# Kernel optimization log

Hardware: AMD Instinct MI355X
Metric: run time of the kernel (lower is better)

Reference implementation:

```python
import jax, jax.numpy as jnp
import numpy as np
import itertools
from jax import lax

B, CIN, COUT, RES, NH = 32, 512, 512, 56, 8
STRIDE = RES // 7  # 8 -> post-stride grid is 7x7 (N=49)
HD = COUT // NH    # 64


def _affine(x, s, b):  # BatchNorm2d in inference form (per-channel scale/shift)
    return x * s[None, :, None, None] + b[None, :, None, None]


def _conv1x1(x, w):  # w: [O, C]
    return jnp.einsum('oc,bchw->bohw', w, x)


def _conv3x3(x, w, stride, groups):
    return lax.conv_general_dilated(
        x, w, window_strides=(stride, stride), padding=[(1, 1), (1, 1)],
        feature_group_count=groups, dimension_numbers=('NCHW', 'OIHW', 'NCHW'))


def _bias_idx():
    points = list(itertools.product(range(7), range(7)))
    offsets, idxs = {}, []
    for p1 in points:
        for p2 in points:
            off = (abs(p1[0] - p2[0]), abs(p1[1] - p2[1]))
            if off not in offsets:
                offsets[off] = len(offsets)
            idxs.append(offsets[off])
    return np.array(idxs, dtype=np.int32).reshape(49, 49), len(offsets)


def setup_inputs() -> dict:
    key = jax.random.key(0)
    ks = jax.random.split(key, 24)
    idx_np, n_off = _bias_idx()  # n_off = 49
    rn = lambda k, sh, sc: jax.random.normal(k, sh, dtype=jnp.float32) * sc
    return {
        'x': rn(ks[0], (B, CIN, RES, RES), 1.0),
        'dw_w': rn(ks[1], (CIN, 1, 3, 3), 0.2),
        'bn0_s': 1.0 + rn(ks[2], (CIN,), 0.05), 'bn0_b': rn(ks[3], (CIN,), 0.05),
        'wq': rn(ks[4], (COUT, CIN), 0.03),
        'bnq_s': 1.0 + rn(ks[5], (COUT,), 0.05), 'bnq_b': rn(ks[6], (COUT,), 0.05),
        'wk': rn(ks[7], (COUT, CIN), 0.03),
        'bnk_s': 1.0 + rn(ks[8], (COUT,), 0.05), 'bnk_b': rn(ks[9], (COUT,), 0.05),
        'wv': rn(ks[10], (COUT, CIN), 0.03),
        'bnv_s': 1.0 + rn(ks[11], (COUT,), 0.05), 'bnv_b': rn(ks[12], (COUT,), 0.05),
        'loc_w': rn(ks[13], (COUT, COUT // NH, 3, 3), 0.05), 'loc_b': rn(ks[14], (COUT,), 0.02),
        'bnl_s': 1.0 + rn(ks[15], (COUT,), 0.05), 'bnl_b': rn(ks[16], (COUT,), 0.05),
        'th1': rn(ks[17], (NH, NH), 0.3), 'th2': rn(ks[18], (NH, NH), 0.3),
        'logit_scale': jnp.log(10.0) * jnp.ones((NH, 1, 1), dtype=jnp.float32),
        'ab': rn(ks[19], (NH, n_off), 0.02),
        'wo': rn(ks[20], (COUT, COUT), 0.03),
        'bno_s': 1.0 + rn(ks[21], (COUT,), 0.05), 'bno_b': rn(ks[22], (COUT,), 0.05),
        'bias_idx': jnp.array(idx_np),
    }


def reference(x, dw_w, bn0_s, bn0_b, wq, bnq_s, bnq_b, wk, bnk_s, bnk_b,
              wv, bnv_s, bnv_b, loc_w, loc_b, bnl_s, bnl_b, th1, th2,
              logit_scale, ab, wo, bno_s, bno_b, bias_idx):
    # stride_conv: depthwise 3x3 stride-8 + BN -> [B, C, 7, 7]
    x = _affine(_conv3x3(x, dw_w, STRIDE, CIN), bn0_s, bn0_b)
    Bc, C, H, W = x.shape
    N = H * W  # 49
    q = _affine(_conv1x1(x, wq), bnq_s, bnq_b).reshape(Bc, NH, HD, N).transpose(0, 1, 3, 2)  # [B,H,N,d]
    k = _affine(_conv1x1(x, wk), bnk_s, bnk_b).reshape(Bc, NH, HD, N)                        # [B,H,d,N]
    v4 = _affine(_conv1x1(x, wv), bnv_s, bnv_b)                                              # [B,Cout,7,7]
    v_local = _affine(_conv3x3(v4, loc_w, 1, NH) + loc_b[None, :, None, None], bnl_s, bnl_b)
    v = v4.reshape(Bc, NH, HD, N).transpose(0, 1, 3, 2)                                      # [B,H,N,d]
    # faithful to source: q normalized over head_dim, k normalized over token axis (last)
    qn = q / jnp.maximum(jnp.linalg.norm(q, axis=-1, keepdims=True), 1e-12)
    kn = k / jnp.maximum(jnp.linalg.norm(k, axis=-1, keepdims=True), 1e-12)
    ls = jnp.exp(jnp.minimum(logit_scale, jnp.log(100.0)))  # clamp max then exp
    attn = jnp.einsum('bhnd,bhdm->bhnm', qn, kn) * ls + ab[:, bias_idx]  # [B,H,49,49]
    attn = jnp.einsum('ij,bjnm->binm', th1, attn)   # talking head 1
    attn = jax.nn.softmax(attn, axis=-1)
    attn = jnp.einsum('ij,bjnm->binm', th2, attn)   # talking head 2
    out = jnp.einsum('bhnm,bhmd->bhnd', attn, v)    # [B,H,N,d]
    out = out.transpose(0, 1, 3, 2).reshape(Bc, COUT, H, W) + v_local
    out = jax.image.resize(out, (Bc, COUT, H * STRIDE, W * STRIDE), method='bilinear')
    out = out * jax.nn.relu6(out + 3.0) / 6.0       # Hardswish
    return _affine(_conv1x1(out, wo), bno_s, bno_b)
```

## Files before the change

kernel.cpp:

```cpp
#include <hip/hip_runtime.h>
#include <hip/hip_bf16.h>
#include <stdint.h>

typedef short short8 __attribute__((ext_vector_type(8)));
typedef float f32x4 __attribute__((ext_vector_type(4)));

#define NB    32
#define NC    512
#define NHD   8
#define HDD   64
#define N7    49
#define RES   56
#define P56   3136
#define NTOK  1568
#define NTOKP 1664
#define NBIG  100352
#define KDIM  512
#define KLOC  576

__device__ __forceinline__ void gload_lds16(const __hip_bfloat16* g, __hip_bfloat16* l) {
  __builtin_amdgcn_global_load_lds(
      (const __attribute__((address_space(1))) void*)g,
      (__attribute__((address_space(3))) void*)l, 16, 0, 0);
}

__global__ __launch_bounds__(256) void k_stride_cvt(
    const float* __restrict__ x, const float* __restrict__ dw,
    const float* __restrict__ s0, const float* __restrict__ b0,
    __hip_bfloat16* __restrict__ xs,
    const float* __restrict__ c0, const float* __restrict__ c1,
    const float* __restrict__ c2, const float* __restrict__ c3,
    const float* __restrict__ c4,
    __hip_bfloat16* __restrict__ d0, __hip_bfloat16* __restrict__ d1,
    __hip_bfloat16* __restrict__ d2, __hip_bfloat16* __restrict__ d3,
    __hip_bfloat16* __restrict__ d4) {
  const int bid = blockIdx.x, t = threadIdx.x;
  if (bid >= 4096) {
    const long base = (long)(bid - 4096) * 2048;
#pragma unroll
    for (int j = 0; j < 8; ++j) {
      long i = base + t + j * 256;
      const float* s; __hip_bfloat16* d; long off;
      if (i >= 1048576)      { s = c4; d = d4; off = i - 1048576; }
      else if (i >= 786432)  { s = c3; d = d3; off = i - 786432; }
      else if (i >= 524288)  { s = c2; d = d2; off = i - 524288; }
      else if (i >= 262144)  { s = c1; d = d1; off = i - 262144; }
      else                   { s = c0; d = d0; off = i; }
      d[off] = __float2bfloat16(s[off]);
    }
    return;
  }
  const int b = bid >> 7, cig = bid & 127;
  const int sub = t >> 6, lane = t & 63;
  const int ci = cig * 4 + sub;
  __shared__ float rows[4][21][56];
  const float* xp = x + ((size_t)(b * NC + ci)) * RES * RES;
  for (int r = lane; r < 21 * 56; r += 64) {
    int rr = r / 56, cc = r - rr * 56;
    int oh = rr / 3, kh = rr - oh * 3;
    int ih = oh * 8 + kh - 1;
    rows[sub][rr][cc] = (ih >= 0) ? xp[ih * 56 + cc] : 0.f;
  }
  float w[9];
#pragma unroll
  for (int j = 0; j < 9; ++j) w[j] = dw[ci * 9 + j];
  const float sc = s0[ci], bi = b0[ci];
  __syncthreads();
  if (lane < 49) {
    const int oh = lane / 7, ow = lane - oh * 7;
    float acc = 0.f;
#pragma unroll
    for (int kh = 0; kh < 3; ++kh)
#pragma unroll
      for (int kw = 0; kw < 3; ++kw) {
        int col = ow * 8 + kw - 1;
        float v = (col >= 0) ? rows[sub][oh * 3 + kh][col] : 0.f;
        acc += v * w[kh * 3 + kw];
      }
    xs[(size_t)(b * 49 + lane) * NC + ci] = __float2bfloat16(acc * sc + bi);
  }
}

__global__ __launch_bounds__(512) void k_gemm_big(
    const __hip_bfloat16* __restrict__ A,
    const __hip_bfloat16* __restrict__ Bm,
    const float* __restrict__ scale, const float* __restrict__ bias,
    float* __restrict__ out) {
  __shared__ __align__(16) __hip_bfloat16 lsA[4][256 * 32];
  __shared__ __align__(16) __hip_bfloat16 lsB[4][256 * 32];
  const int t = threadIdx.x;
  const int cpx = gridDim.x >> 3;
  const int nid = (blockIdx.x & 7) * cpx + (blockIdx.x >> 3);
  const int m0 = (nid & 1) * 256, n0 = (nid >> 1) * 256;

  const int lane = t & 63, wid = t >> 6;
  const int wm = (wid >> 2) * 128, wn = (wid & 3) * 64;
  const int fr = lane & 15, fq = lane >> 4;
  const int rslot = (fq ^ ((fr >> 1) & 3)) * 8;

  const int srow = t >> 2;
  const int scol = ((t & 3) ^ ((t >> 3) & 3)) * 8;
  const __hip_bfloat16* Ab = A  + (size_t)(m0 + srow) * KDIM + scol;
  const __hip_bfloat16* Bb = Bm + (size_t)(n0 + srow) * KDIM + scol;

  const f32x4 fz = {0.f, 0.f, 0.f, 0.f};
  f32x4 acc[8][4];
#pragma unroll
  for (int i = 0; i < 8; ++i)
#pragma unroll
    for (int j = 0; j < 4; ++j) acc[i][j] = fz;

#define STA(tile, call) gload_lds16(Ab + (tile) * 32 + (size_t)(call) * 128 * KDIM, \
                                    lsA[(tile) & 3] + (call) * 4096 + wid * 512)
#define STB(tile, call) gload_lds16(Bb + (tile) * 32 + (size_t)(call) * 128 * KDIM, \
                                    lsB[(tile) & 3] + (call) * 4096 + wid * 512)

  STA(0, 0); STA(0, 1); STB(0, 0); STB(0, 1);
  STA(1, 0); STA(1, 1); STB(1, 0); STB(1, 1);
  asm volatile("s_waitcnt vmcnt(4)" ::: "memory");
  __builtin_amdgcn_sched_barrier(0);
  __builtin_amdgcn_s_barrier();
  __builtin_amdgcn_sched_barrier(0);

#pragma unroll 1
  for (int tt = 0; tt < 16; ++tt) {
    const __hip_bfloat16* lA = lsA[tt & 3];
    const __hip_bfloat16* lB = lsB[tt & 3];
    const int ft = tt + 2;

    short8 af[4], bf[4], ag[4];
#pragma unroll
    for (int i = 0; i < 4; ++i)
      af[i] = *(const short8*)(lA + (wm + i * 16 + fr) * 32 + rslot);
#pragma unroll
    for (int j = 0; j < 4; ++j)
      bf[j] = *(const short8*)(lB + (wn + j * 16 + fr) * 32 + rslot);
    if (ft < 16) { STA(ft, 0); STA(ft, 1); }
    __builtin_amdgcn_sched_barrier(0);
    __builtin_amdgcn_s_barrier();
    asm volatile("s_waitcnt lgkmcnt(0)" ::: "memory");
    __builtin_amdgcn_sched_barrier(0);
    __builtin_amdgcn_s_setprio(1);
#pragma unroll
    for (int i = 0; i < 4; ++i)
#pragma unroll
      for (int j = 0; j < 4; ++j)
        acc[i][j] = __builtin_amdgcn_mfma_f32_16x16x32_bf16(af[i], bf[j], acc[i][j], 0, 0, 0);
    __builtin_amdgcn_s_setprio(0);
    __builtin_amdgcn_sched_barrier(0);
    __builtin_amdgcn_s_barrier();
    __builtin_amdgcn_sched_barrier(0);

#pragma unroll
    for (int i = 0; i < 4; ++i)
      ag[i] = *(const short8*)(lA + (wm + 64 + i * 16 + fr) * 32 + rslot);
    if (ft < 16) { STB(ft, 0); STB(ft, 1); }
    __builtin_amdgcn_sched_barrier(0);
    __builtin_amdgcn_s_barrier();
    asm volatile("s_waitcnt lgkmcnt(0)" ::: "memory");
    __builtin_amdgcn_sched_barrier(0);
    __builtin_amdgcn_s_setprio(1);
#pragma unroll
    for (int i = 0; i < 4; ++i)
#pragma unroll
      for (int j = 0; j < 4; ++j)
        acc[4 + i][j] = __builtin_amdgcn_mfma_f32_16x16x32_bf16(ag[i], bf[j], acc[4 + i][j], 0, 0, 0);
    __builtin_amdgcn_s_setprio(0);
    __builtin_amdgcn_sched_barrier(0);

    if (tt < 14)      asm volatile("s_waitcnt vmcnt(4)" ::: "memory");
    else if (tt == 14) asm volatile("s_waitcnt vmcnt(0)" ::: "memory");
    __builtin_amdgcn_sched_barrier(0);
    __builtin_amdgcn_s_barrier();
    __builtin_amdgcn_sched_barrier(0);
  }
#undef STA
#undef STB

#pragma unroll
  for (int mi = 0; mi < 8; ++mi) {
#pragma unroll
    for (int ni = 0; ni < 4; ++ni) {
      const int gn = n0 + wn + ni * 16 + fr;
      const int outer = gn / P56;
      const int ii = gn - outer * P56;
#pragma unroll
      for (int r = 0; r < 4; ++r) {
        const int co = m0 + wm + mi * 16 + fq * 4 + r;
        out[((size_t)outer * NC + co) * P56 + ii] = acc[mi][ni][r] * scale[co] + bias[co];
      }
    }
  }
}

__global__ __launch_bounds__(256) void k_gemm_qkv(
    const __hip_bfloat16* __restrict__ wqb, const __hip_bfloat16* __restrict__ wkb,
    const __hip_bfloat16* __restrict__ wvb, const __hip_bfloat16* __restrict__ xs,
    const float* __restrict__ sq, const float* __restrict__ bq,
    const float* __restrict__ sk, const float* __restrict__ bk,
    const float* __restrict__ sv, const float* __restrict__ bv,
    float* __restrict__ qb, float* __restrict__ kb, float* __restrict__ vb) {
  __shared__ __align__(16) __hip_bfloat16 lsA[2][128 * 32];
  __shared__ __align__(16) __hip_bfloat16 lsB[2][128 * 32];
  const int t = threadIdx.x;
  const int nwg = gridDim.x;
  const int orig = blockIdx.x;
  const int q = nwg >> 3, r = nwg & 7;
  const int xcd = orig & 7, pos = orig >> 3;
  const int nid = (xcd < r ? xcd * (q + 1) : r * (q + 1) + (xcd - r) * q) + pos;
  const int mt = nid % 12, nt = nid / 12;
  const int n0 = nt * 128, m0 = (mt & 3) * 128, sel = mt >> 2;

  const __hip_bfloat16* A = (sel == 0 ? wqb : sel == 1 ? wkb : wvb);
  const float* scale = (sel == 0 ? sq : sel == 1 ? sk : sv);
  const float* bias  = (sel == 0 ? bq : sel == 1 ? bk : bv);
  float* out = (sel == 0 ? qb : sel == 1 ? kb : vb);

  const int lane = t & 63, wid = t >> 6;
  const int wm = (wid >> 1) * 64, wn = (wid & 1) * 64;
  const int fr = lane & 15, fq = lane >> 4;
  const int rslot = (fq ^ ((fr >> 1) & 3)) * 8;
  const int srow = t >> 2;
  const int scol = ((t & 3) ^ ((t >> 3) & 3)) * 8;
  const __hip_bfloat16* Ab = A  + (size_t)(m0 + srow) * KDIM + scol;
  const __hip_bfloat16* Bb = xs + (size_t)(n0 + srow) * KDIM + scol;

  const f32x4 fz = {0.f, 0.f, 0.f, 0.f};
  f32x4 acc[4][4];
#pragma unroll
  for (int i = 0; i < 4; ++i)
#pragma unroll
    for (int j = 0; j < 4; ++j) acc[i][j] = fz;

#define STG_QKV(tile)                                                   \
  do {                                                                  \
    const int kof = (tile) * 32; const int bb = (tile) & 1;             \
    gload_lds16(Ab + kof,                       lsA[bb] + wid * 512);   \
    gload_lds16(Ab + kof + (size_t)64 * KDIM,   lsA[bb] + 2048 + wid * 512); \
    gload_lds16(Bb + kof,                       lsB[bb] + wid * 512);   \
    gload_lds16(Bb + kof + (size_t)64 * KDIM,   lsB[bb] + 2048 + wid * 512); \
  } while (0)

  STG_QKV(0);
  STG_QKV(1);
#pragma unroll 1
  for (int it = 0; it < 16; ++it) {
    if (it < 15) asm volatile("s_waitcnt vmcnt(4)" ::: "memory");
    else         asm volatile("s_waitcnt vmcnt(0)" ::: "memory");
    __builtin_amdgcn_sched_barrier(0);
    __builtin_amdgcn_s_barrier();
    __builtin_amdgcn_sched_barrier(0);
    const __hip_bfloat16* lA = lsA[it & 1];
    const __hip_bfloat16* lB = lsB[it & 1];
    short8 af[4], bf[4];
#pragma unroll
    for (int mi = 0; mi < 4; ++mi)
      af[mi] = *(const short8*)(lA + (wm + mi * 16 + fr) * 32 + rslot);
#pragma unroll
    for (int ni = 0; ni < 4; ++ni)
      bf[ni] = *(const short8*)(lB + (wn + ni * 16 + fr) * 32 + rslot);
#pragma unroll
    for (int mi = 0; mi < 4; ++mi)
#pragma unroll
      for (int ni = 0; ni < 4; ++ni)
        acc[mi][ni] = __builtin_amdgcn_mfma_f32_16x16x32_bf16(af[mi], bf[ni], acc[mi][ni], 0, 0, 0);
    __builtin_amdgcn_sched_barrier(0);
    __builtin_amdgcn_s_barrier();
    __builtin_amdgcn_sched_barrier(0);
    if (it < 14) STG_QKV(it + 2);
  }
#undef STG_QKV

#pragma unroll
  for (int mi = 0; mi < 4; ++mi) {
#pragma unroll
    for (int ni = 0; ni < 4; ++ni) {
      const int gn = n0 + wn + ni * 16 + fr;
      if (gn >= NTOK) continue;
      const int b = gn / 49, ii = gn - b * 49;
#pragma unroll
      for (int r = 0; r < 4; ++r) {
        const int co = m0 + wm + mi * 16 + fq * 4 + r;
        out[((size_t)b * NC + co) * 49 + ii] = acc[mi][ni][r] * scale[co] + bias[co];
      }
    }
  }
}

__global__ __launch_bounds__(256) void k_im2col(
    const float* __restrict__ vb, __hip_bfloat16* __restrict__ bloc) {
  const int g = blockIdx.x, b = blockIdx.y, t = threadIdx.x;
  __shared__ __hip_bfloat16 pad[64][81];
  for (int i = t; i < 64 * 81; i += 256) pad[i / 81][i % 81] = __float2bfloat16(0.f);
  __syncthreads();
  const float* src = vb + ((size_t)b * NC + g * 64) * 49;
  for (int i = t; i < 64 * 49; i += 256) {
    const int ci = i / 49, n = i - ci * 49;
    const int oh = n / 7, ow = n - oh * 7;
    pad[ci][(oh + 1) * 9 + (ow + 1)] = __float2bfloat16(src[i]);
  }
  __syncthreads();
  __hip_bfloat16* dst = bloc + ((size_t)g * NTOKP + (size_t)b * 49) * KLOC;
  for (int i = t; i < 49 * KLOC; i += 256) {
    const int n = i / KLOC, k = i - n * KLOC;
    const int ci = k / 9, tap = k - ci * 9;
    const int kh = tap / 3, kw = tap - kh * 3;
    const int oh = n / 7, ow = n - oh * 7;
    dst[i] = pad[ci][(oh + kh) * 9 + (ow + kw)];
  }
}

__global__ __launch_bounds__(256) void k_vloc_gemm(
    const __hip_bfloat16* __restrict__ lwb,
    const __hip_bfloat16* __restrict__ bloc,
    const float* __restrict__ lbias, const float* __restrict__ sl,
    const float* __restrict__ bl, float* __restrict__ vloc) {
  __shared__ __align__(16) __hip_bfloat16 lsA[2][64 * 32];
  __shared__ __align__(16) __hip_bfloat16 lsB[2][128 * 32];
  const int t = threadIdx.x;
  const int g = blockIdx.y;
  const int n0 = blockIdx.x * 128;
  const int lane = t & 63, wid = t >> 6;
  const int wm = (wid >> 1) * 32, wn = (wid & 1) * 64;
  const int fr = lane & 15, fq = lane >> 4;
  const int rslot = (fq ^ ((fr >> 1) & 3)) * 8;
  const int srow = t >> 2;
  const int scol = ((t & 3) ^ ((t >> 3) & 3)) * 8;
  const __hip_bfloat16* Ab = lwb  + ((size_t)g * 64 + srow) * KLOC + scol;
  const __hip_bfloat16* Bb = bloc + ((size_t)g * NTOKP + n0 + srow) * KLOC + scol;

  const f32x4 fz = {0.f, 0.f, 0.f, 0.f};
  f32x4 acc[2][4];
#pragma unroll
  for (int i = 0; i < 2; ++i)
#pragma unroll
    for (int j = 0; j < 4; ++j) acc[i][j] = fz;

#define STG_VL(tile)                                                     \
  do {                                                                   \
    const int kof = (tile) * 32; const int bb = (tile) & 1;              \
    gload_lds16(Ab + kof,                      lsA[bb] + wid * 512);     \
    gload_lds16(Bb + kof,                      lsB[bb] + wid * 512);     \
    gload_lds16(Bb + kof + (size_t)64 * KLOC,  lsB[bb] + 2048 + wid * 512); \
  } while (0)

  STG_VL(0);
  STG_VL(1);
#pragma unroll 1
  for (int it = 0; it < 18; ++it) {
    if (it < 17) asm volatile("s_waitcnt vmcnt(3)" ::: "memory");
    else         asm volatile("s_waitcnt vmcnt(0)" ::: "memory");
    __builtin_amdgcn_sched_barrier(0);
    __builtin_amdgcn_s_barrier();
    __builtin_amdgcn_sched_barrier(0);
    const __hip_bfloat16* lA = lsA[it & 1];
    const __hip_bfloat16* lB = lsB[it & 1];
    short8 af[2], bf[4];
#pragma unroll
    for (int mi = 0; mi < 2; ++mi)
      af[mi] = *(const short8*)(lA + (wm + mi * 16 + fr) * 32 + rslot);
#pragma unroll
    for (int ni = 0; ni < 4; ++ni)
      bf[ni] = *(const short8*)(lB + (wn + ni * 16 + fr) * 32 + rslot);
#pragma unroll
    for (int mi = 0; mi < 2; ++mi)
#pragma unroll
      for (int ni = 0; ni < 4; ++ni)
        acc[mi][ni] = __builtin_amdgcn_mfma_f32_16x16x32_bf16(af[mi], bf[ni], acc[mi][ni], 0, 0, 0);
    __builtin_amdgcn_sched_barrier(0);
    __builtin_amdgcn_s_barrier();
    __builtin_amdgcn_sched_barrier(0);
    if (it < 16) STG_VL(it + 2);
  }
#undef STG_VL

#pragma unroll
  for (int mi = 0; mi < 2; ++mi) {
#pragma unroll
    for (int ni = 0; ni < 4; ++ni) {
      const int gn = n0 + wn + ni * 16 + fr;
      if (gn >= NTOK) continue;
      const int b = gn / 49, n = gn - b * 49;
#pragma unroll
      for (int r = 0; r < 4; ++r) {
        const int oc = g * 64 + wm + mi * 16 + fq * 4 + r;
        const float sc = sl[oc];
        vloc[((size_t)b * NC + oc) * 49 + n] = acc[mi][ni][r] * sc + lbias[oc] * sc + bl[oc];
      }
    }
  }
}

__global__ __launch_bounds__(256) void k_attn1(
    const float* __restrict__ qb, const float* __restrict__ kb,
    const float* __restrict__ lsc, const float* __restrict__ ab, const int* __restrict__ bidx,
    float* __restrict__ Sbuf) {
  const int h = blockIdx.x, b = blockIdx.y, t = threadIdx.x;
  __shared__ float qt[64 * 49], kt[64 * 49], nq[49], abl[49];
  const float* qs = qb + ((size_t)b * NC + h * 64) * 49;
  const float* ks = kb + ((size_t)b * NC + h * 64) * 49;
  for (int i = t; i < 64 * 49; i += 256) { qt[i] = qs[i]; kt[i] = ks[i]; }
  if (t < 49) abl[t] = ab[h * 49 + t];
  __syncthreads();
  if (t < 49) {
    float s = 0.f;
    for (int d = 0; d < 64; ++d) { float v = qt[d * 49 + t]; s += v * v; }
    nq[t] = fmaxf(sqrtf(s), 1e-12f);
  } else if (t >= 64 && t < 128) {
    const int d = t - 64;
    float s = 0.f;
    for (int m = 0; m < 49; ++m) { float v = kt[d * 49 + m]; s += v * v; }
    const float inv = 1.f / fmaxf(sqrtf(s), 1e-12f);
    for (int m = 0; m < 49; ++m) kt[d * 49 + m] *= inv;
  }
  __syncthreads();
  const float ls = expf(fminf(lsc[h], logf(100.f)));
  for (int idx = t; idx < 49 * 49; idx += 256) {
    const int n = idx / 49, m = idx - n * 49;
    float acc = 0.f;
    for (int d = 0; d < 64; ++d) acc += qt[d * 49 + n] * kt[d * 49 + m];
    Sbuf[(((size_t)b * NHD + h) * 49 + n) * 49 + m] = acc / nq[n] * ls + abl[bidx[idx]];
  }
}

__global__ __launch_bounds__(256) void k_attn2(
    const float* __restrict__ Sbuf, const float* __restrict__ th1, const float* __restrict__ th2,
    const float* __restrict__ vb, const float* __restrict__ vloc, float* __restrict__ y7) {
  const int n = blockIdx.x, b = blockIdx.y, t = threadIdx.x;
  __shared__ float sS[8][49], sP[8][49], sQ[8][49];
  __shared__ float t1[64], t2[64], rsuminv[8];
  if (t < 64) { t1[t] = th1[t]; t2[t] = th2[t]; }
  for (int i = t; i < 392; i += 256) {
    const int j = i / 49, m = i - j * 49;
    sS[j][m] = Sbuf[(((size_t)b * NHD + j) * 49 + n) * 49 + m];
  }
  __syncthreads();
  for (int i = t; i < 392; i += 256) {
    const int j = i / 49, m = i - j * 49;
    float a = 0.f;
#pragma unroll
    for (int jj = 0; jj < 8; ++jj) a += t1[j * 8 + jj] * sS[jj][m];
    sP[j][m] = a;
  }
  __syncthreads();
  if (t < 8) {
    float mx = -1e30f;
    for (int m = 0; m < 49; ++m) mx = fmaxf(mx, sP[t][m]);
    float s = 0.f;
    for (int m = 0; m < 49; ++m) { float e = expf(sP[t][m] - mx); sP[t][m] = e; s += e; }
    rsuminv[t] = 1.f / s;
  }
  __syncthreads();
  for (int i = t; i < 392; i += 256) {
    const int j = i / 49, m = i - j * 49;
    float a = 0.f;
#pragma unroll
    for (int jj = 0; jj < 8; ++jj) a += t2[j * 8 + jj] * (sP[jj][m] * rsuminv[jj]);
    sQ[j][m] = a;
  }
  __syncthreads();
  for (int c = t; c < NC; c += 256) {
    const int hh = c >> 6;
    const float* vp = vb + ((size_t)b * NC + c) * 49;
    float a = 0.f;
    for (int m = 0; m < 49; ++m) a += sQ[hh][m] * vp[m];
    a += vloc[((size_t)b * NC + c) * 49 + n];
    y7[((size_t)b * 49 + n) * NC + c] = a;
  }
}

__global__ __launch_bounds__(256) void k_resize(const float* __restrict__ y7,
                                                __hip_bfloat16* __restrict__ h) {
  const int y = blockIdx.x, b = blockIdx.y, t = threadIdx.x;
  __shared__ float L[2][7][512];
  float sy = (y - 3.5f) * 0.125f;
  sy = fminf(fmaxf(sy, 0.f), 6.f);
  const int iy0 = min((int)floorf(sy), 5);
  const float wy = sy - (float)iy0;
  const float* src = y7 + ((size_t)b * 49 + iy0 * 7) * NC;
  float* Lf = &L[0][0][0];
  for (int i = t; i < 2 * 7 * 512; i += 256) Lf[i] = src[i];
  __syncthreads();
  const size_t outb = ((size_t)b * P56 + (size_t)y * 56) * NC;
  const int c0 = t * 2;
  for (int x = 0; x < 56; ++x) {
    float sx = (x - 3.5f) * 0.125f;
    sx = fminf(fmaxf(sx, 0.f), 6.f);
    const int ix0 = min((int)floorf(sx), 5);
    const float wx = sx - (float)ix0;
    const float w00 = (1.f - wy) * (1.f - wx), w01 = (1.f - wy) * wx;
    const float w10 = wy * (1.f - wx),         w11 = wy * wx;
    float hs[2];
#pragma unroll
    for (int j = 0; j < 2; ++j) {
      const int c = c0 + j;
      const float v = w00 * L[0][ix0][c] + w01 * L[0][ix0 + 1][c]
                    + w10 * L[1][ix0][c] + w11 * L[1][ix0 + 1][c];
      hs[j] = v * fminf(fmaxf(v + 3.f, 0.f), 6.f) * (1.f / 6.f);
    }
    __hip_bfloat162 p;
    p.x = __float2bfloat16(hs[0]);
    p.y = __float2bfloat16(hs[1]);
    *(__hip_bfloat162*)(&h[outb + (size_t)x * NC + c0]) = p;
  }
}

extern "C" void kernel_launch(void* const* d_in, const int* in_sizes, int n_in,
                              void* d_out, int out_size, void* d_ws, size_t ws_size,
                              hipStream_t stream) {
  (void)in_sizes; (void)n_in; (void)out_size; (void)ws_size;
  const float* x     = (const float*)d_in[0];
  const float* dw_w  = (const float*)d_in[1];
  const float* bn0_s = (const float*)d_in[2];
  const float* bn0_b = (const float*)d_in[3];
  const float* wq    = (const float*)d_in[4];
  const float* bnq_s = (const float*)d_in[5];
  const float* bnq_b = (const float*)d_in[6];
  const float* wk    = (const float*)d_in[7];
  const float* bnk_s = (const float*)d_in[8];
  const float* bnk_b = (const float*)d_in[9];
  const float* wv    = (const float*)d_in[10];
  const float* bnv_s = (const float*)d_in[11];
  const float* bnv_b = (const float*)d_in[12];
  const float* loc_w = (const float*)d_in[13];
  const float* loc_b = (const float*)d_in[14];
  const float* bnl_s = (const float*)d_in[15];
  const float* bnl_b = (const float*)d_in[16];
  const float* th1   = (const float*)d_in[17];
  const float* th2   = (const float*)d_in[18];
  const float* lsc   = (const float*)d_in[19];
  const float* ab    = (const float*)d_in[20];
  const float* wo    = (const float*)d_in[21];
  const float* bno_s = (const float*)d_in[22];
  const float* bno_b = (const float*)d_in[23];
  const int*   bidx  = (const int*)d_in[24];

  char* w = (char*)d_ws;
  auto alloc = [&](size_t bytes) {
    char* p = w;
    w += (bytes + 255) & ~(size_t)255;
    return p;
  };
  __hip_bfloat16* h_buf = (__hip_bfloat16*)alloc((size_t)NBIG * NC * 2);
  __hip_bfloat16* wq_b  = (__hip_bfloat16*)alloc((size_t)NC * NC * 2);
  __hip_bfloat16* wk_b  = (__hip_bfloat16*)alloc((size_t)NC * NC * 2);
  __hip_bfloat16* wv_b  = (__hip_bfloat16*)alloc((size_t)NC * NC * 2);
  __hip_bfloat16* wo_b  = (__hip_bfloat16*)alloc((size_t)NC * NC * 2);
  __hip_bfloat16* lw_b  = (__hip_bfloat16*)alloc((size_t)NC * KLOC * 2);
  __hip_bfloat16* xs    = (__hip_bfloat16*)alloc((size_t)NTOKP * NC * 2);
  float* qb   = (float*)alloc((size_t)NB * NC * 49 * 4);
  float* kb   = (float*)alloc((size_t)NB * NC * 49 * 4);
  float* vb   = (float*)alloc((size_t)NB * NC * 49 * 4);
  float* vloc = (float*)alloc((size_t)NB * NC * 49 * 4);
  float* y7   = (float*)alloc((size_t)NB * 49 * NC * 4);
  float* Sb   = (float*)alloc((size_t)NB * NHD * 49 * 49 * 4);
  __hip_bfloat16* bloc = (__hip_bfloat16*)h_buf;

  k_stride_cvt<<<dim3(4096 + 656), 256, 0, stream>>>(
      x, dw_w, bn0_s, bn0_b, xs,
      wq, wk, wv, wo, loc_w, wq_b, wk_b, wv_b, wo_b, lw_b);
  k_gemm_qkv<<<dim3(13 * 12), 256, 0, stream>>>(wq_b, wk_b, wv_b, xs,
                                                bnq_s, bnq_b, bnk_s, bnk_b, bnv_s, bnv_b,
                                                qb, kb, vb);
  k_im2col<<<dim3(NHD, NB), 256, 0, stream>>>(vb, bloc);
  k_vloc_gemm<<<dim3(13, NHD), 256, 0, stream>>>(lw_b, bloc, loc_b, bnl_s, bnl_b, vloc);
  k_attn1<<<dim3(NHD, NB), 256, 0, stream>>>(qb, kb, lsc, ab, bidx, Sb);
  k_attn2<<<dim3(49, NB), 256, 0, stream>>>(Sb, th1, th2, vb, vloc, y7);
  k_resize<<<dim3(RES, NB), 256, 0, stream>>>(y7, h_buf);
  k_gemm_big<<<dim3(784), 512, 0, stream>>>(wo_b, h_buf, bno_s, bno_b, (float*)d_out);
}
```

Measured before the change: 262.5 us.

## Simplify GEMM pipeline to one barrier per K-tile and vectorize resize stores

The GEMM main loop drops its multi-phase barrier schedule. It now uses a single wait and barrier at the top of each K-step, issues all prefetches for tile tt+2 at once, and loads every A/B fragment before running all 32 MFMAs. The intent is to cut barrier and lgkmcnt stalls per iteration, at the cost of holding more fragment registers live. The resize kernel now has each thread produce 8 channels and write 16-byte bf16 stores instead of 2-element stores, spreading x positions across thread groups.

```diff
diff --git a/kernel.cpp b/kernel.cpp
--- a/kernel.cpp
+++ b/kernel.cpp
@@ -117,62 +117,40 @@
 
   STA(0, 0); STA(0, 1); STB(0, 0); STB(0, 1);
   STA(1, 0); STA(1, 1); STB(1, 0); STB(1, 1);
-  asm volatile("s_waitcnt vmcnt(4)" ::: "memory");
-  __builtin_amdgcn_sched_barrier(0);
-  __builtin_amdgcn_s_barrier();
-  __builtin_amdgcn_sched_barrier(0);
 
 #pragma unroll 1
   for (int tt = 0; tt < 16; ++tt) {
+    if (tt < 15) asm volatile("s_waitcnt vmcnt(4)" ::: "memory");
+    else         asm volatile("s_waitcnt vmcnt(0)" ::: "memory");
+    __builtin_amdgcn_sched_barrier(0);
+    __builtin_amdgcn_s_barrier();
+    __builtin_amdgcn_sched_barrier(0);
+    if (tt < 14) { STA(tt + 2, 0); STA(tt + 2, 1); STB(tt + 2, 0); STB(tt + 2, 1); }
+
     const __hip_bfloat16* lA = lsA[tt & 3];
     const __hip_bfloat16* lB = lsB[tt & 3];
-    const int ft = tt + 2;
-
-    short8 af[4], bf[4], ag[4];
+    short8 af[4], ag[4], bf[4];
 #pragma unroll
     for (int i = 0; i < 4; ++i)
       af[i] = *(const short8*)(lA + (wm + i * 16 + fr) * 32 + rslot);
 #pragma unroll
+    for (int i = 0; i < 4; ++i)
+      ag[i] = *(const short8*)(lA + (wm + 64 + i * 16 + fr) * 32 + rslot);
+#pragma unroll
     for (int j = 0; j < 4; ++j)
       bf[j] = *(const short8*)(lB + (wn + j * 16 + fr) * 32 + rslot);
-    if (ft < 16) { STA(ft, 0); STA(ft, 1); }
-    __builtin_amdgcn_sched_barrier(0);
-    __builtin_amdgcn_s_barrier();
-    asm volatile("s_waitcnt lgkmcnt(0)" ::: "memory");
-    __builtin_amdgcn_sched_barrier(0);
     __builtin_amdgcn_s_setprio(1);
 #pragma unroll
     for (int i = 0; i < 4; ++i)
 #pragma unroll
       for (int j = 0; j < 4; ++j)
         acc[i][j] = __builtin_amdgcn_mfma_f32_16x16x32_bf16(af[i], bf[j], acc[i][j], 0, 0, 0);
-    __builtin_amdgcn_s_setprio(0);
-    __builtin_amdgcn_sched_barrier(0);
-    __builtin_amdgcn_s_barrier();
-    __builtin_amdgcn_sched_barrier(0);
-
-#pragma unroll
-    for (int i = 0; i < 4; ++i)
-      ag[i] = *(const short8*)(lA + (wm + 64 + i * 16 + fr) * 32 + rslot);
-    if (ft < 16) { STB(ft, 0); STB(ft, 1); }
-    __builtin_amdgcn_sched_barrier(0);
-    __builtin_amdgcn_s_barrier();
-    asm volatile("s_waitcnt lgkmcnt(0)" ::: "memory");
-    __builtin_amdgcn_sched_barrier(0);
-    __builtin_amdgcn_s_setprio(1);
 #pragma unroll
     for (int i = 0; i < 4; ++i)
 #pragma unroll
       for (int j = 0; j < 4; ++j)
         acc[4 + i][j] = __builtin_amdgcn_mfma_f32_16x16x32_bf16(ag[i], bf[j], acc[4 + i][j], 0, 0, 0);
     __builtin_amdgcn_s_setprio(0);
-    __builtin_amdgcn_sched_barrier(0);
-
-    if (tt < 14)      asm volatile("s_waitcnt vmcnt(4)" ::: "memory");
-    else if (tt == 14) asm volatile("s_waitcnt vmcnt(0)" ::: "memory");
-    __builtin_amdgcn_sched_barrier(0);
-    __builtin_amdgcn_s_barrier();
-    __builtin_amdgcn_sched_barrier(0);
   }
 #undef STA
 #undef STB
@@ -482,26 +460,26 @@
   for (int i = t; i < 2 * 7 * 512; i += 256) Lf[i] = src[i];
   __syncthreads();
   const size_t outb = ((size_t)b * P56 + (size_t)y * 56) * NC;
-  const int c0 = t * 2;
-  for (int x = 0; x < 56; ++x) {
+  const int cg = (t & 63) * 8;
+  const int xq = t >> 6;
+  for (int x0 = 0; x0 < 56; x0 += 4) {
+    const int x = x0 + xq;
     float sx = (x - 3.5f) * 0.125f;
     sx = fminf(fmaxf(sx, 0.f), 6.f);
     const int ix0 = min((int)floorf(sx), 5);
     const float wx = sx - (float)ix0;
     const float w00 = (1.f - wy) * (1.f - wx), w01 = (1.f - wy) * wx;
     const float w10 = wy * (1.f - wx),         w11 = wy * wx;
-    float hs[2];
-#pragma unroll
-    for (int j = 0; j < 2; ++j) {
-      const int c = c0 + j;
+    short8 pk;
+#pragma unroll
+    for (int j = 0; j < 8; ++j) {
+      const int c = cg + j;
       const float v = w00 * L[0][ix0][c] + w01 * L[0][ix0 + 1][c]
                     + w10 * L[1][ix0][c] + w11 * L[1][ix0 + 1][c];
-      hs[j] = v * fminf(fmaxf(v + 3.f, 0.f), 6.f) * (1.f / 6.f);
+      const float hs = v * fminf(fmaxf(v + 3.f, 0.f), 6.f) * (1.f / 6.f);
+      pk[j] = (short)__bfloat16_as_ushort(__float2bfloat16(hs));
     }
-    __hip_bfloat162 p;
-    p.x = __float2bfloat16(hs[0]);
-    p.y = __float2bfloat16(hs[1]);
-    *(__hip_bfloat162*)(&h[outb + (size_t)x * NC + c0]) = p;
+    *(short8*)(&h[outb + (size_t)x * NC + cg]) = pk;
   }
 }
 
```

After: 265.1 us. Within noise of the previous version (+1.0%).
